# Kernel tuning notes

Hardware: AMD Instinct MI355X
Metric: run time of the kernel (lower is better)

The kernel has to match this reference:

```python
import jax, jax.numpy as jnp
import numpy as np
import math

S, B, D_MODEL = 1024, 2, 1024
N_HEADS = 16
D_HEAD = D_MODEL // N_HEADS
C = 32  # compressed_len


def _xavier(key, shape):
    fan_in, fan_out = shape[-1], shape[-2] if len(shape) > 1 else shape[-1]
    limit = math.sqrt(6.0 / (fan_in + fan_out))
    return jax.random.uniform(key, shape, jnp.float32, -limit, limit)


def setup_inputs() -> dict:
    key = jax.random.key(0)
    ks = jax.random.split(key, 10)
    return {
        "x": jax.random.normal(ks[0], (S, B, D_MODEL), jnp.float32),
        "q_down": _xavier(ks[1], (C, D_MODEL)),
        "Wq": _xavier(ks[2], (D_MODEL, D_MODEL)),
        "bq": jnp.zeros((D_MODEL,), jnp.float32),
        "Wk": _xavier(ks[3], (D_MODEL, D_MODEL)),
        "bk": jnp.zeros((D_MODEL,), jnp.float32),
        "Wv": _xavier(ks[4], (D_MODEL, D_MODEL)),
        "bv": jnp.zeros((D_MODEL,), jnp.float32),
        "Wo": _xavier(ks[5], (D_MODEL, D_MODEL)),
        "bo": jnp.zeros((D_MODEL,), jnp.float32),
    }


def reference(x, q_down, Wq, bq, Wk, bk, Wv, bv, Wo, bo):
    # x: (s, b, d_model); causal=True, rope=None, dropout inactive (eval)
    s, b, d_model = x.shape
    h, dh = N_HEADS, D_HEAD
    scale = 1.0 / math.sqrt(dh)

    q_u = x @ Wq.T + bq                       # (s,b,dm)
    k_d = x @ Wk.T + bk
    v_d = x @ Wv.T + bv
    v_d_k = v_d @ Wk.T + bk
    v_d_v = v_d @ Wv.T + bv

    def heads(t):  # (s,b,dm) -> (b,h,s,dh)
        return t.reshape(s, b, h, dh).transpose(1, 2, 0, 3)

    q_u = heads(q_u) * scale
    k_d = heads(k_d)
    v_d_kv = jnp.concatenate([heads(v_d_k), heads(v_d_v)], axis=-1)  # (b,h,s,2dh)

    q_d = q_down.reshape(C, h, dh).transpose(1, 0, 2) * scale        # (h,c,dh)

    down = jnp.einsum('hcd,bhsd->bhcs', q_d, k_d)                    # (b,h,c,s)
    w = jnp.exp(down - jnp.max(down, axis=-1, keepdims=True))
    norm = jnp.cumsum(w, axis=-1)

    # (b,h,c,s,2dh): running compressed KV state
    kv_u = jnp.cumsum(w[..., None] * v_d_kv[:, :, None, :, :], axis=3) / norm[..., None]
    k_u, v_u = jnp.split(kv_u, 2, axis=-1)                           # each (b,h,c,s,dh)

    up = jnp.einsum('bhsd,bhcsd->bhsc', q_u, k_u)
    up = jax.nn.softmax(up, axis=-1)
    out = jnp.einsum('bhsc,bhcsd->bhsd', up, v_u)                    # (b,h,s,dh)

    out = out.transpose(2, 0, 1, 3).reshape(s, b, d_model)
    return out @ Wo.T + bo
```

## Files before the change

### kernel.cpp

```cpp
#include <hip/hip_runtime.h>
#include <cstdint>
#include <cstddef>

#define S_LEN 1024
#define BATCH 2
#define DM    1024
#define NH    16
#define DH    64
#define CC    32
#define SB    2048
#define TSD   128
#define NCHD  8

using short8 = __attribute__((ext_vector_type(8))) short;
using f32x4  = __attribute__((ext_vector_type(4))) float;

__device__ __forceinline__ float b2f(unsigned short u) {
    union { unsigned int i; float f; } v; v.i = ((unsigned int)u) << 16; return v.f;
}
__device__ __forceinline__ unsigned short f2b(float f) {
    union { float f; unsigned int i; } v; v.f = f;
    unsigned int x = v.i;
    unsigned int r = x + 0x7FFFu + ((x >> 16) & 1u);
    return (unsigned short)(r >> 16);
}

__device__ __forceinline__ void async_ld16(const unsigned short* g, unsigned short* l) {
    __builtin_amdgcn_global_load_lds(
        (const __attribute__((address_space(1))) unsigned int*)g,
        (__attribute__((address_space(3))) unsigned int*)l,
        16, 0, 0);
}

__global__ __launch_bounds__(256) void k_convert(
    const void* x, const void* qd,
    const void* wq, const void* wk, const void* wv,
    const void* bq, const void* bk, const void* bv, const void* bo,
    int* __restrict__ flag,
    unsigned short* xb, unsigned short* qdb,
    unsigned short* Wqb, unsigned short* Wkb, unsigned short* Wvb,
    float* biasf)
{
    __shared__ int cnt;
    if (threadIdx.x == 0) cnt = 0;
    __syncthreads();
    {
        const unsigned short* xs = (const unsigned short*)x;
        int local = 0;
        for (int i = threadIdx.x; i < 1024; i += 256) {
            unsigned e = (xs[i * 2] >> 7) & 0xFF;
            if (e >= 90 && e <= 160) local++;
        }
        atomicAdd(&cnt, local);
    }
    __syncthreads();
    const int isbf = (cnt >= 640);
    if (blockIdx.x == 0 && threadIdx.x == 0) *flag = isbf;

    const size_t tid = (size_t)blockIdx.x * 256 + threadIdx.x;
    const size_t stride = (size_t)gridDim.x * 256;

    if (!isbf) {
        auto cv = [&](const void* src, unsigned short* dst, size_t n) {
            const float4* s = (const float4*)src;
            for (size_t i = tid; i < n / 4; i += stride) {
                float4 v = s[i];
                ushort4 o;
                o.x = f2b(v.x); o.y = f2b(v.y); o.z = f2b(v.z); o.w = f2b(v.w);
                ((ushort4*)dst)[i] = o;
            }
        };
        cv(x,  xb,  (size_t)SB * DM);
        cv(qd, qdb, (size_t)CC * DM);
        cv(wq, Wqb, (size_t)DM * DM);
        cv(wk, Wkb, (size_t)DM * DM);
        cv(wv, Wvb, (size_t)DM * DM);
    }
    for (size_t i = tid; i < 5 * DM; i += stride) {
        int w = (int)(i >> 10), o = (int)(i & 1023);
        float val;
        if (w == 4) val = 0.f;
        else {
            const void* bp = (w == 0) ? bq : ((w == 1) ? bk : ((w == 2) ? bv : bo));
            val = isbf ? b2f(((const unsigned short*)bp)[o]) : ((const float*)bp)[o];
        }
        biasf[i] = val;
    }
}

struct GArg {
    const unsigned short* A0;
    const unsigned short* A1;
    const unsigned short* B0;
    const unsigned short* B1;
    const float* bias;
    void* out;
    float scale;
    int mode;
};

__global__ __launch_bounds__(256) void k_g1conv(
    GArg g0, GArg g1, GArg g2, const int* __restrict__ flag,
    int M, int N, int K,
    const void* __restrict__ wo_raw, unsigned short* __restrict__ Wob)
{
    const int isbf = *flag;
    const int t = threadIdx.x;

    if (blockIdx.z == 3) {
        if (!isbf) {
            const float4* s = (const float4*)wo_raw;
            const int id = blockIdx.y * 8 + blockIdx.x;
            for (int i = id * 256 + t; i < (DM * DM) / 4; i += 256 * 256) {
                float4 v = s[i];
                ushort4 o;
                o.x = f2b(v.x); o.y = f2b(v.y); o.z = f2b(v.z); o.w = f2b(v.w);
                ((ushort4*)Wob)[i] = o;
            }
        }
        return;
    }

    GArg ga = (blockIdx.z == 0) ? g0 : (blockIdx.z == 1) ? g1 : g2;
    const unsigned short* Ap = isbf ? ga.A1 : ga.A0;
    const unsigned short* Bp = isbf ? ga.B1 : ga.B0;
    const int m0 = blockIdx.y * 64;
    const int n0 = blockIdx.x * 128;
    __shared__ __align__(16) unsigned short As[2][64 * 32];
    __shared__ __align__(16) unsigned short Bs[2][128 * 32];
    const int w = t >> 6, l = t & 63;
    const int wm = w >> 1, wn = w & 1;
    const int lr = l >> 2;
    const int lk = (l & 3) * 8;
    const int ln = l & 15;
    const int lq = l >> 4;

    f32x4 acc[2][4] = {};

    const unsigned short* Ab  = Ap + (size_t)(m0 + w * 16 +      lr) * K + lk;
    const unsigned short* Bb0 = Bp + (size_t)(n0 + w * 32 +      lr) * K + lk;
    const unsigned short* Bb1 = Bp + (size_t)(n0 + w * 32 + 16 + lr) * K + lk;

    for (int kk = 0; kk < K; kk += 64) {
#pragma unroll
        for (int hh = 0; hh < 2; ++hh) {
            async_ld16(Ab  + kk + hh * 32, &As[hh][w * 512]);
            async_ld16(Bb0 + kk + hh * 32, &Bs[hh][w * 1024]);
            async_ld16(Bb1 + kk + hh * 32, &Bs[hh][w * 1024 + 512]);
        }
        __syncthreads();
#pragma unroll
        for (int hh = 0; hh < 2; ++hh) {
            short8 af[2], bfr[4];
#pragma unroll
            for (int i = 0; i < 2; ++i)
                af[i] = *(const short8*)&As[hh][(wm * 32 + i * 16 + ln) * 32 + lq * 8];
#pragma unroll
            for (int j = 0; j < 4; ++j)
                bfr[j] = *(const short8*)&Bs[hh][(wn * 64 + j * 16 + ln) * 32 + lq * 8];
#pragma unroll
            for (int i = 0; i < 2; ++i)
#pragma unroll
                for (int j = 0; j < 4; ++j)
                    acc[i][j] = __builtin_amdgcn_mfma_f32_16x16x32_bf16(af[i], bfr[j], acc[i][j], 0, 0, 0);
        }
        __syncthreads();
    }

    const float sc = ga.scale;
#pragma unroll
    for (int j = 0; j < 4; ++j) {
        int col = n0 + wn * 64 + j * 16 + ln;
        float bv = ga.bias[col];
#pragma unroll
        for (int i = 0; i < 2; ++i) {
            int row0 = m0 + wm * 32 + i * 16 + lq * 4;
#pragma unroll
            for (int r = 0; r < 4; ++r) {
                float v = (acc[i][j][r] + bv) * sc;
                ((unsigned short*)ga.out)[(size_t)(row0 + r) * N + col] = f2b(v);
            }
        }
    }
}

__global__ __launch_bounds__(256) void gemm_f64(GArg ga,
                                                const int* __restrict__ flag,
                                                int M, int N, int K)
{
    const int isbf = *flag;
    const unsigned short* Ap = isbf ? ga.A1 : ga.A0;
    const unsigned short* Bp = isbf ? ga.B1 : ga.B0;
    const int m0 = blockIdx.y * 64;
    const int n0 = blockIdx.x * 64;
    __shared__ __align__(16) unsigned short As[2][64 * 32];
    __shared__ __align__(16) unsigned short Bs[2][64 * 32];
    const int t = threadIdx.x;
    const int w = t >> 6, l = t & 63;
    const int wm = w >> 1, wn = w & 1;
    const int lr = l >> 2;
    const int lk = (l & 3) * 8;
    const int ln = l & 15;
    const int lq = l >> 4;

    f32x4 acc[2][2] = {};

    const unsigned short* Ab = Ap + (size_t)(m0 + w * 16 + lr) * K + lk;
    const unsigned short* Bb = Bp + (size_t)(n0 + w * 16 + lr) * K + lk;

    for (int kk = 0; kk < K; kk += 64) {
#pragma unroll
        for (int hh = 0; hh < 2; ++hh) {
            async_ld16(Ab + kk + hh * 32, &As[hh][w * 512]);
            async_ld16(Bb + kk + hh * 32, &Bs[hh][w * 512]);
        }
        __syncthreads();
#pragma unroll
        for (int hh = 0; hh < 2; ++hh) {
            short8 af[2], bfr[2];
#pragma unroll
            for (int i = 0; i < 2; ++i)
                af[i] = *(const short8*)&As[hh][(wm * 32 + i * 16 + ln) * 32 + lq * 8];
#pragma unroll
            for (int j = 0; j < 2; ++j)
                bfr[j] = *(const short8*)&Bs[hh][(wn * 32 + j * 16 + ln) * 32 + lq * 8];
#pragma unroll
            for (int i = 0; i < 2; ++i)
#pragma unroll
                for (int j = 0; j < 2; ++j)
                    acc[i][j] = __builtin_amdgcn_mfma_f32_16x16x32_bf16(af[i], bfr[j], acc[i][j], 0, 0, 0);
        }
        __syncthreads();
    }

    const int f32o = (ga.mode == 0) ? 1 : (ga.mode == 1) ? 0 : (!isbf);
    const float sc = ga.scale;
#pragma unroll
    for (int j = 0; j < 2; ++j) {
        int col = n0 + wn * 32 + j * 16 + ln;
        float bv = ga.bias[col];
#pragma unroll
        for (int i = 0; i < 2; ++i) {
            int row0 = m0 + wm * 32 + i * 16 + lq * 4;
#pragma unroll
            for (int r = 0; r < 4; ++r) {
                float v = (acc[i][j][r] + bv) * sc;
                size_t idx = (size_t)(row0 + r) * N + col;
                if (f32o) ((float*)ga.out)[idx] = v;
                else      ((unsigned short*)ga.out)[idx] = f2b(v);
            }
        }
    }
}

__global__ __launch_bounds__(256) void k_g2down(
    GArg g0, GArg g1, const int* __restrict__ flag, int M, int N, int K,
    const unsigned short* __restrict__ kd,
    const unsigned short* __restrict__ qd0,
    const unsigned short* __restrict__ qd1,
    float* __restrict__ wbuf,
    float* __restrict__ cmax,
    float* __restrict__ csum)
{
    __shared__ __align__(16) unsigned char SM[40448];
    const int isbf = *flag;
    const int t = threadIdx.x;
    const int w = t >> 6, l = t & 63;
    const int ln = l & 15, lq = l >> 4;

    if (blockIdx.z < 2) {
        unsigned short* As = (unsigned short*)SM;
        unsigned short* Bs = (unsigned short*)(SM + 8192);
        GArg ga = blockIdx.z ? g1 : g0;
        const unsigned short* Ap = isbf ? ga.A1 : ga.A0;
        const unsigned short* Bp = isbf ? ga.B1 : ga.B0;
        const int m0 = blockIdx.y * 64;
        const int n0 = blockIdx.x * 128;
        const int wm = w >> 1, wn = w & 1;
        const int lr = l >> 2;
        const int lk = (l & 3) * 8;

        f32x4 acc[2][4] = {};

        const unsigned short* Ab  = Ap + (size_t)(m0 + w * 16 +      lr) * K + lk;
        const unsigned short* Bb0 = Bp + (size_t)(n0 + w * 32 +      lr) * K + lk;
        const unsigned short* Bb1 = Bp + (size_t)(n0 + w * 32 + 16 + lr) * K + lk;

        for (int kk = 0; kk < K; kk += 64) {
#pragma unroll
            for (int hh = 0; hh < 2; ++hh) {
                async_ld16(Ab  + kk + hh * 32, &As[hh * 2048 + w * 512]);
                async_ld16(Bb0 + kk + hh * 32, &Bs[hh * 4096 + w * 1024]);
                async_ld16(Bb1 + kk + hh * 32, &Bs[hh * 4096 + w * 1024 + 512]);
            }
            __syncthreads();
#pragma unroll
            for (int hh = 0; hh < 2; ++hh) {
                short8 af[2], bfr[4];
#pragma unroll
                for (int i = 0; i < 2; ++i)
                    af[i] = *(const short8*)&As[hh * 2048 + (wm * 32 + i * 16 + ln) * 32 + lq * 8];
#pragma unroll
                for (int j = 0; j < 4; ++j)
                    bfr[j] = *(const short8*)&Bs[hh * 4096 + (wn * 64 + j * 16 + ln) * 32 + lq * 8];
#pragma unroll
                for (int i = 0; i < 2; ++i)
#pragma unroll
                    for (int j = 0; j < 4; ++j)
                        acc[i][j] = __builtin_amdgcn_mfma_f32_16x16x32_bf16(af[i], bfr[j], acc[i][j], 0, 0, 0);
            }
            __syncthreads();
        }

        const float sc = ga.scale;
#pragma unroll
        for (int j = 0; j < 4; ++j) {
            int col = n0 + wn * 64 + j * 16 + ln;
            float bv = ga.bias[col];
#pragma unroll
            for (int i = 0; i < 2; ++i) {
                int row0 = m0 + wm * 32 + i * 16 + lq * 4;
#pragma unroll
                for (int r = 0; r < 4; ++r) {
                    float v = (acc[i][j][r] + bv) * sc;
                    ((unsigned short*)ga.out)[(size_t)(row0 + r) * N + col] = f2b(v);
                }
            }
        }
    } else {
        unsigned short* QD = (unsigned short*)SM;
        unsigned short* KT = (unsigned short*)(SM + 4608);
        float* SS          = (float*)(SM + 23040);
        float* cmf         = (float*)(SM + 39936);

        const int id = blockIdx.y * 8 + blockIdx.x;
        const unsigned short* qdw = isbf ? qd1 : qd0;
        const int bh = id >> 3;
        const int b = bh >> 4, h = bh & 15;
        const int chunk = id & 7;
        const int s0 = chunk * TSD;

        {
            int r = t >> 3, cb = (t & 7) * 8;
            *(short8*)&QD[r * 72 + cb] = *(const short8*)&qdw[(size_t)r * DM + h * DH + cb];
        }
        for (int u = t; u < 128 * 8; u += 256) {
            int r = u >> 3, cb = (u & 7) * 8;
            *(short8*)&KT[r * 72 + cb] =
                *(const short8*)&kd[(size_t)((s0 + r) * BATCH + b) * DM + h * DH + cb];
        }
        __syncthreads();

        f32x4 accG[2][2] = {};
#pragma unroll
        for (int ks = 0; ks < 2; ++ks) {
            short8 a8[2], b8[2];
#pragma unroll
            for (int i = 0; i < 2; ++i)
                a8[i] = *(const short8*)&QD[(i * 16 + ln) * 72 + ks * 32 + lq * 8];
#pragma unroll
            for (int j = 0; j < 2; ++j)
                b8[j] = *(const short8*)&KT[(w * 32 + j * 16 + ln) * 72 + ks * 32 + lq * 8];
#pragma unroll
            for (int i = 0; i < 2; ++i)
#pragma unroll
                for (int j = 0; j < 2; ++j)
                    accG[i][j] = __builtin_amdgcn_mfma_f32_16x16x32_bf16(a8[i], b8[j], accG[i][j], 0, 0, 0);
        }
#pragma unroll
        for (int i = 0; i < 2; ++i) {
#pragma unroll
            for (int j = 0; j < 2; ++j) {
                int sl = w * 32 + j * 16 + ln;
#pragma unroll
                for (int r = 0; r < 4; ++r) {
                    int c = i * 16 + lq * 4 + r;
                    float v = accG[i][j][r] * 0.125f;
                    SS[c * 132 + sl] = v;
                    wbuf[((size_t)bh * CC + c) * S_LEN + s0 + sl] = v;
                }
            }
        }
        __syncthreads();

        const int c = t >> 3, sub = t & 7;
        float lmax = -3.4e38f;
#pragma unroll
        for (int k = 0; k < 16; ++k) lmax = fmaxf(lmax, SS[c * 132 + sub * 16 + k]);
        lmax = fmaxf(lmax, __shfl_xor(lmax, 1));
        lmax = fmaxf(lmax, __shfl_xor(lmax, 2));
        lmax = fmaxf(lmax, __shfl_xor(lmax, 4));
        if (sub == 0) {
            cmf[c] = lmax;
            cmax[((size_t)bh * CC + c) * NCHD + chunk] = lmax;
        }
        __syncthreads();
        const float cm = cmf[c];
        float es = 0.f;
#pragma unroll
        for (int k = 0; k < 16; ++k) es += __expf(SS[c * 132 + sub * 16 + k] - cm);
        es += __shfl_xor(es, 1);
        es += __shfl_xor(es, 2);
        es += __shfl_xor(es, 4);
        if (sub == 0) csum[((size_t)bh * CC + c) * NCHD + chunk] = es;
    }
}

__global__ __launch_bounds__(256) void k_wstate(
    const float* __restrict__ wbuf,
    const float* __restrict__ cmax,
    const float* __restrict__ csum,
    const unsigned short* __restrict__ vdk,
    const unsigned short* __restrict__ vdv,
    unsigned short* __restrict__ wb,
    float* __restrict__ invn,
    float* __restrict__ Mst,
    float* __restrict__ NTst)
{
    __shared__ __align__(16) unsigned char SM[45568];
    unsigned short* Wfull = (unsigned short*)SM;
    unsigned char* R = SM + 8704;
    float* gm    = (float*)R;
    float* basep = (float*)(R + 128);
    float* psum  = (float*)(R + 256);
    float* invt  = (float*)(R + 1408);
    unsigned short* T1 = (unsigned short*)R;
    unsigned short* T2 = (unsigned short*)(R + 9216);
    unsigned short* KT = (unsigned short*)(R + 18432);
    unsigned short* VT = (unsigned short*)(R + 27648);

    const int bh = blockIdx.x, seg = blockIdx.y;
    const int b = bh >> 4, h = bh & 15;
    const int t = threadIdx.x;
    const int w = t >> 6, l = t & 63;
    const int ln = l & 15, lq = l >> 4;

    if (t < CC) {
        const size_t cb = (size_t)(bh * CC + t) * NCHD;
        float m = cmax[cb];
#pragma unroll
        for (int g = 1; g < NCHD; ++g) m = fmaxf(m, cmax[cb + g]);
        gm[t] = m;
        float bsum = 0.f;
        for (int k = 0; k < seg; ++k)
            bsum += csum[cb + k] * __expf(cmax[cb + k] - m);
        basep[t] = bsum;
    }
    __syncthreads();

    {
        const int c = t >> 3, sub = t & 7;
        const float gmc = gm[c];
        const size_t rbase = (size_t)bh * 32768 + c * 1024 + seg * 128 + sub * 16;
        float w16[16];
        float s = 0.f;
#pragma unroll
        for (int i = 0; i < 16; ++i) {
            float v = __expf(wbuf[rbase + i] - gmc);
            w16[i] = v; s += v;
        }
        psum[c * 9 + sub] = s;
        short8 o0, o1;
#pragma unroll
        for (int i = 0; i < 8; ++i) { o0[i] = f2b(w16[i]); o1[i] = f2b(w16[8 + i]); }
        *(short8*)&wb[rbase] = o0;
        *(short8*)&wb[rbase + 8] = o1;
        *(short8*)&Wfull[c * 136 + sub * 16] = o0;
        *(short8*)&Wfull[c * 136 + sub * 16 + 8] = o1;
        __syncthreads();

        float run = basep[c];
        for (int k = 0; k < sub; ++k) run += psum[c * 9 + k];
#pragma unroll
        for (int i = 0; i < 16; ++i) {
            run += w16[i];
            invt[(sub * 16 + i) * 36 + c] = 1.0f / fmaxf(run, 1e-30f);
        }
    }
    __syncthreads();

    for (int u = t; u < 128 * 8; u += 256) {
        int r = u >> 3, cb2 = (u & 7) * 4;
        *(float4*)&invn[(size_t)bh * 32768 + (seg * 128 + r) * 32 + cb2] =
            *(const float4*)&invt[r * 36 + cb2];
    }
    __syncthreads();

    for (int rep = 0; rep < 2; ++rep) {
        const int ch = seg * 2 + rep;
        const int s0 = ch * 64;

        for (int u = t; u < 64 * 8; u += 256) {
            int r = u >> 3, cb = (u & 7) * 8;
            *(short8*)&T1[r * 72 + cb] =
                *(const short8*)&vdk[(size_t)((s0 + r) * BATCH + b) * DM + h * DH + cb];
            *(short8*)&T2[r * 72 + cb] =
                *(const short8*)&vdv[(size_t)((s0 + r) * BATCH + b) * DM + h * DH + cb];
        }
        __syncthreads();
        for (int u = t; u < 64 * 8; u += 256) {
            int d = u >> 3, s8 = (u & 7) * 8;
            short8 o1, o2;
#pragma unroll
            for (int k = 0; k < 8; ++k) {
                o1[k] = T1[(s8 + k) * 72 + d];
                o2[k] = T2[(s8 + k) * 72 + d];
            }
            *(short8*)&KT[d * 72 + s8] = o1;
            *(short8*)&VT[d * 72 + s8] = o2;
        }
        __syncthreads();

        f32x4 accM[2] = {};
#pragma unroll
        for (int ks = 0; ks < 2; ++ks) {
            short8 b8 = *(const short8*)&KT[(w * 16 + ln) * 72 + ks * 32 + lq * 8];
#pragma unroll
            for (int i = 0; i < 2; ++i) {
                short8 a8 = *(const short8*)&Wfull[(i * 16 + ln) * 136 + rep * 64 + ks * 32 + lq * 8];
                accM[i] = __builtin_amdgcn_mfma_f32_16x16x32_bf16(a8, b8, accM[i], 0, 0, 0);
            }
        }
#pragma unroll
        for (int i = 0; i < 2; ++i)
#pragma unroll
            for (int r = 0; r < 4; ++r)
                Mst[((size_t)(bh * 16 + ch) * 32 + i * 16 + lq * 4 + r) * 64 + w * 16 + ln] = accM[i][r];

        f32x4 accN[2] = {};
#pragma unroll
        for (int ks = 0; ks < 2; ++ks) {
            short8 a8 = *(const short8*)&VT[(w * 16 + ln) * 72 + ks * 32 + lq * 8];
#pragma unroll
            for (int j = 0; j < 2; ++j) {
                short8 b8 = *(const short8*)&Wfull[(j * 16 + ln) * 136 + rep * 64 + ks * 32 + lq * 8];
                accN[j] = __builtin_amdgcn_mfma_f32_16x16x32_bf16(a8, b8, accN[j], 0, 0, 0);
            }
        }
#pragma unroll
        for (int j = 0; j < 2; ++j)
#pragma unroll
            for (int r = 0; r < 4; ++r)
                NTst[((size_t)(bh * 16 + ch) * 64 + w * 16 + lq * 4 + r) * 32 + j * 16 + ln] = accN[j][r];
        __syncthreads();
    }
}

__global__ __launch_bounds__(256) void k_att(
    const unsigned short* __restrict__ qu,
    const unsigned short* __restrict__ vdk,
    const unsigned short* __restrict__ wb,
    const float* __restrict__ invn,
    const unsigned short* __restrict__ vdv,
    const float* __restrict__ Mst,
    const float* __restrict__ NTst,
    unsigned short* __restrict__ attout)
{
    const int bh = blockIdx.x, b = bh >> 4, h = bh & 15;
    const int qi = blockIdx.y;
    const int s0 = qi * 64;
    const int t = threadIdx.x;
    const int w = t >> 6, l = t & 63;
    const int wy = w >> 1, wx = w & 1;
    const int ln = l & 15, lq = l >> 4;

    __shared__ __align__(16) unsigned short Qs[64 * 72];
    __shared__ __align__(16) unsigned short Gs[64 * 72];
    __shared__ __align__(16) unsigned short Kd[64 * 72];
    __shared__ __align__(16) unsigned short Wd[32 * 72];
    __shared__ __align__(16) unsigned short WTd[64 * 40];
    __shared__ __align__(16) unsigned short VTd[64 * 72];
    __shared__ __align__(16) unsigned short Mc[32 * 72];
    __shared__ __align__(16) unsigned short Nc[64 * 40];

    for (int u = t; u < 64 * 8; u += 256) {
        int r = u >> 3, cb = (u & 7) * 8;
        *(short8*)&Qs[r * 72 + cb] =
            *(const short8*)&qu[(size_t)(s0 + r) * 2048 + b * 1024 + h * 64 + cb];
        *(short8*)&Kd[r * 72 + cb] =
            *(const short8*)&vdk[(size_t)(s0 + r) * 2048 + b * 1024 + h * 64 + cb];
        *(short8*)&Gs[r * 72 + cb] =
            *(const short8*)&vdv[(size_t)(s0 + r) * 2048 + b * 1024 + h * 64 + cb];
    }
    for (int u = t; u < 32 * 8; u += 256) {
        int r = u >> 3, cb = (u & 7) * 8;
        *(short8*)&Wd[r * 72 + cb] =
            *(const short8*)&wb[(size_t)bh * 32768 + r * 1024 + s0 + cb];
    }
    {
        float am[8] = {0.f, 0.f, 0.f, 0.f, 0.f, 0.f, 0.f, 0.f};
        float an[8] = {0.f, 0.f, 0.f, 0.f, 0.f, 0.f, 0.f, 0.f};
        for (int ch = 0; ch < qi; ++ch) {
            const float* pm = Mst + ((size_t)(bh * 16 + ch)) * 2048 + t * 8;
            const float* pn = NTst + ((size_t)(bh * 16 + ch)) * 2048 + t * 8;
            float4 m0 = *(const float4*)pm;
            float4 m1 = *(const float4*)(pm + 4);
            float4 n0 = *(const float4*)pn;
            float4 n1 = *(const float4*)(pn + 4);
            am[0] += m0.x; am[1] += m0.y; am[2] += m0.z; am[3] += m0.w;
            am[4] += m1.x; am[5] += m1.y; am[6] += m1.z; am[7] += m1.w;
            an[0] += n0.x; an[1] += n0.y; an[2] += n0.z; an[3] += n0.w;
            an[4] += n1.x; an[5] += n1.y; an[6] += n1.z; an[7] += n1.w;
        }
        short8 mo, no;
#pragma unroll
        for (int j = 0; j < 8; ++j) { mo[j] = f2b(am[j]); no[j] = f2b(an[j]); }
        *(short8*)&Mc[(t >> 3) * 72 + (t & 7) * 8] = mo;
        *(short8*)&Nc[(t >> 2) * 40 + (t & 3) * 8] = no;
    }
    __syncthreads();

    for (int u = t; u < 64 * 8; u += 256) {
        int d = u >> 3, s8 = (u & 7) * 8;
        short8 o;
#pragma unroll
        for (int k = 0; k < 8; ++k) o[k] = Gs[(s8 + k) * 72 + d];
        *(short8*)&VTd[d * 72 + s8] = o;
    }
    {
        int sl = t >> 2, cb = (t & 3) * 8;
        short8 o;
#pragma unroll
        for (int k = 0; k < 8; ++k) o[k] = Wd[(cb + k) * 72 + sl];
        *(short8*)&WTd[sl * 40 + cb] = o;
    }
    __syncthreads();

    {
        f32x4 accG[2][2] = {};
#pragma unroll
        for (int ks = 0; ks < 2; ++ks) {
            short8 a8[2], b8[2];
#pragma unroll
            for (int i = 0; i < 2; ++i)
                a8[i] = *(const short8*)&Qs[(wy * 32 + i * 16 + ln) * 72 + ks * 32 + lq * 8];
#pragma unroll
            for (int j = 0; j < 2; ++j)
                b8[j] = *(const short8*)&Kd[(wx * 32 + j * 16 + ln) * 72 + ks * 32 + lq * 8];
#pragma unroll
            for (int i = 0; i < 2; ++i)
#pragma unroll
                for (int j = 0; j < 2; ++j)
                    accG[i][j] = __builtin_amdgcn_mfma_f32_16x16x32_bf16(a8[i], b8[j], accG[i][j], 0, 0, 0);
        }
        __syncthreads();
#pragma unroll
        for (int i = 0; i < 2; ++i) {
            int row = wy * 32 + i * 16 + lq * 4;
#pragma unroll
            for (int j = 0; j < 2; ++j) {
                int col = wx * 32 + j * 16 + ln;
#pragma unroll
                for (int r = 0; r < 4; ++r) {
                    float v = accG[i][j][r];
                    if (col > row + r) v = 0.f;
                    Gs[(row + r) * 72 + col] = f2b(v);
                }
            }
        }
    }
    __syncthreads();

    f32x4 accU[2] = {};
#pragma unroll
    for (int ks = 0; ks < 2; ++ks) {
        short8 ga = *(const short8*)&Gs[(w * 16 + ln) * 72 + ks * 32 + lq * 8];
        short8 qa = *(const short8*)&Qs[(w * 16 + ln) * 72 + ks * 32 + lq * 8];
#pragma unroll
        for (int j = 0; j < 2; ++j) {
            short8 wf = *(const short8*)&Wd[(j * 16 + ln) * 72 + ks * 32 + lq * 8];
            short8 mf = *(const short8*)&Mc[(j * 16 + ln) * 72 + ks * 32 + lq * 8];
            accU[j] = __builtin_amdgcn_mfma_f32_16x16x32_bf16(ga, wf, accU[j], 0, 0, 0);
            accU[j] = __builtin_amdgcn_mfma_f32_16x16x32_bf16(qa, mf, accU[j], 0, 0, 0);
        }
    }
    __syncthreads();

    {
        int rowl = w * 16 + lq * 4;
#pragma unroll
        for (int r = 0; r < 4; ++r) {
            int srow = s0 + rowl + r;
            float inv0 = invn[(size_t)bh * 32768 + srow * 32 + ln];
            float inv1 = invn[(size_t)bh * 32768 + srow * 32 + 16 + ln];
            float l0 = accU[0][r] * inv0;
            float l1 = accU[1][r] * inv1;
            float m = fmaxf(l0, l1);
#pragma unroll
            for (int msk = 1; msk < 16; msk <<= 1) m = fmaxf(m, __shfl_xor(m, msk));
            float e0 = __expf(l0 - m), e1 = __expf(l1 - m);
            float Z = e0 + e1;
#pragma unroll
            for (int msk = 1; msk < 16; msk <<= 1) Z += __shfl_xor(Z, msk);
            float iz = 1.0f / Z;
            Qs[(rowl + r) * 40 + ln]      = f2b(e0 * iz * inv0);
            Qs[(rowl + r) * 40 + 16 + ln] = f2b(e1 * iz * inv1);
        }
    }
    __syncthreads();

    short8 pa[2];
#pragma unroll
    for (int i = 0; i < 2; ++i)
        pa[i] = *(const short8*)&Qs[(wy * 32 + i * 16 + ln) * 40 + lq * 8];
    {
        f32x4 accS[2][2] = {};
        short8 b8[2];
#pragma unroll
        for (int j = 0; j < 2; ++j)
            b8[j] = *(const short8*)&WTd[(wx * 32 + j * 16 + ln) * 40 + lq * 8];
#pragma unroll
        for (int i = 0; i < 2; ++i)
#pragma unroll
            for (int j = 0; j < 2; ++j)
                accS[i][j] = __builtin_amdgcn_mfma_f32_16x16x32_bf16(pa[i], b8[j], accS[i][j], 0, 0, 0);
#pragma unroll
        for (int i = 0; i < 2; ++i) {
            int row = wy * 32 + i * 16 + lq * 4;
#pragma unroll
            for (int j = 0; j < 2; ++j) {
                int col = wx * 32 + j * 16 + ln;
#pragma unroll
                for (int r = 0; r < 4; ++r) {
                    float v = accS[i][j][r];
                    if (col > row + r) v = 0.f;
                    Gs[(row + r) * 72 + col] = f2b(v);
                }
            }
        }
    }
    __syncthreads();

    {
        f32x4 accO[2][2] = {};
        short8 n8[2];
#pragma unroll
        for (int j = 0; j < 2; ++j)
            n8[j] = *(const short8*)&Nc[(wx * 32 + j * 16 + ln) * 40 + lq * 8];
#pragma unroll
        for (int i = 0; i < 2; ++i)
#pragma unroll
            for (int j = 0; j < 2; ++j)
                accO[i][j] = __builtin_amdgcn_mfma_f32_16x16x32_bf16(pa[i], n8[j], accO[i][j], 0, 0, 0);
#pragma unroll
        for (int ks = 0; ks < 2; ++ks) {
            short8 a8[2], b8[2];
#pragma unroll
            for (int i = 0; i < 2; ++i)
                a8[i] = *(const short8*)&Gs[(wy * 32 + i * 16 + ln) * 72 + ks * 32 + lq * 8];
#pragma unroll
            for (int j = 0; j < 2; ++j)
                b8[j] = *(const short8*)&VTd[(wx * 32 + j * 16 + ln) * 72 + ks * 32 + lq * 8];
#pragma unroll
            for (int i = 0; i < 2; ++i)
#pragma unroll
                for (int j = 0; j < 2; ++j)
                    accO[i][j] = __builtin_amdgcn_mfma_f32_16x16x32_bf16(a8[i], b8[j], accO[i][j], 0, 0, 0);
        }
#pragma unroll
        for (int i = 0; i < 2; ++i) {
            int rowb = s0 + wy * 32 + i * 16 + lq * 4;
#pragma unroll
            for (int j = 0; j < 2; ++j) {
                int d = wx * 32 + j * 16 + ln;
#pragma unroll
                for (int r = 0; r < 4; ++r)
                    attout[(size_t)(rowb + r) * 2048 + b * 1024 + h * 64 + d] = f2b(accO[i][j][r]);
            }
        }
    }
}

extern "C" void kernel_launch(void* const* d_in, const int* in_sizes, int n_in,
                              void* d_out, int out_size, void* d_ws, size_t ws_size,
                              hipStream_t stream)
{
    (void)in_sizes; (void)n_in; (void)out_size; (void)ws_size;
    char* ws = (char*)d_ws;
    const size_t MB = (size_t)1 << 20;
    const size_t KB = (size_t)1 << 10;
    unsigned short* attout = (unsigned short*)(ws + 0 * MB);
    unsigned short* q_u    = (unsigned short*)(ws + 4 * MB);
    unsigned short* k_d    = (unsigned short*)(ws + 8 * MB);
    unsigned short* v_dk   = (unsigned short*)(ws + 12 * MB);
    unsigned short* v_dv   = (unsigned short*)(ws + 16 * MB);
    float* wbuf = (float*)(ws + 20 * MB);
    unsigned short* wb  = (unsigned short*)(ws + 24 * MB);
    float* invn = (float*)(ws + 28 * MB);
    float* Mst  = (float*)(ws + 32 * MB);
    float* NTst = (float*)(ws + 36 * MB);
    unsigned short* xb  = (unsigned short*)(ws + 44 * MB);
    unsigned short* Wqb = (unsigned short*)(ws + 48 * MB);
    unsigned short* Wkb = (unsigned short*)(ws + 50 * MB);
    unsigned short* Wvb = (unsigned short*)(ws + 52 * MB);
    unsigned short* Wob = (unsigned short*)(ws + 54 * MB);
    unsigned short* v_d = (unsigned short*)(ws + 56 * MB);
    unsigned short* qdb = (unsigned short*)(ws + 62 * MB);
    float* biasf  = (float*)(ws + 62 * MB + 64 * KB);
    float* cmax   = (float*)(ws + 62 * MB + 192 * KB);
    float* csum   = (float*)(ws + 62 * MB + 256 * KB);
    int*   flag   = (int*)  (ws + 62 * MB + 320 * KB);

    const unsigned short* xraw  = (const unsigned short*)d_in[0];
    const unsigned short* qdraw = (const unsigned short*)d_in[1];
    const unsigned short* wqraw = (const unsigned short*)d_in[2];
    const unsigned short* wkraw = (const unsigned short*)d_in[4];
    const unsigned short* wvraw = (const unsigned short*)d_in[6];
    const unsigned short* woraw = (const unsigned short*)d_in[8];

    k_convert<<<1024, 256, 0, stream>>>(
        d_in[0], d_in[1], d_in[2], d_in[4], d_in[6],
        d_in[3], d_in[5], d_in[7], d_in[9],
        flag, xb, qdb, Wqb, Wkb, Wvb, biasf);

    const float* bqf = biasf;
    const float* bkf = biasf + 1024;
    const float* bvf = biasf + 2048;
    const float* bof = biasf + 3072;

    GArg gq { xb, xraw, Wqb, wqraw, bqf, (void*)q_u, 0.125f, 1 };
    GArg gk { xb, xraw, Wkb, wkraw, bkf, (void*)k_d, 1.0f, 1 };
    GArg gv { xb, xraw, Wvb, wvraw, bvf, (void*)v_d, 1.0f, 1 };
    k_g1conv<<<dim3(8, 32, 4), 256, 0, stream>>>(gq, gk, gv, flag, SB, DM, DM,
                                                 d_in[8], Wob);

    GArg gvk{ v_d, v_d, Wkb, wkraw, bkf, (void*)v_dk, 1.0f, 1 };
    GArg gvv{ v_d, v_d, Wvb, wvraw, bvf, (void*)v_dv, 1.0f, 1 };
    k_g2down<<<dim3(8, 32, 3), 256, 0, stream>>>(gvk, gvv, flag, SB, DM, DM,
                                                 k_d, qdb, qdraw, wbuf, cmax, csum);

    k_wstate<<<dim3(32, 8), 256, 0, stream>>>(wbuf, cmax, csum, v_dk, v_dv,
                                              wb, invn, Mst, NTst);
    k_att<<<dim3(32, 16), 256, 0, stream>>>(q_u, v_dk, wb, invn, v_dv,
                                            Mst, NTst, attout);

    GArg go{ attout, attout, Wob, woraw, bof, d_out, 1.0f, 2 };
    gemm_f64<<<dim3(16, 32), 256, 0, stream>>>(go, flag, SB, DM, DM);
}
```

Before: 164.5 us.

## Fuse fp32-to-bf16 input conversion into GEMM tile loads and drop convert kernel

```diff
diff --git a/kernel.cpp b/kernel.cpp
--- a/kernel.cpp
+++ b/kernel.cpp
@@ -32,85 +32,52 @@
         16, 0, 0);
 }
 
-__global__ __launch_bounds__(256) void k_convert(
-    const void* x, const void* qd,
-    const void* wq, const void* wk, const void* wv,
-    const void* bq, const void* bk, const void* bv, const void* bo,
-    int* __restrict__ flag,
-    unsigned short* xb, unsigned short* qdb,
-    unsigned short* Wqb, unsigned short* Wkb, unsigned short* Wvb,
-    float* biasf)
-{
-    __shared__ int cnt;
-    if (threadIdx.x == 0) cnt = 0;
-    __syncthreads();
-    {
-        const unsigned short* xs = (const unsigned short*)x;
-        int local = 0;
-        for (int i = threadIdx.x; i < 1024; i += 256) {
-            unsigned e = (xs[i * 2] >> 7) & 0xFF;
-            if (e >= 90 && e <= 160) local++;
-        }
-        atomicAdd(&cnt, local);
-    }
-    __syncthreads();
-    const int isbf = (cnt >= 640);
-    if (blockIdx.x == 0 && threadIdx.x == 0) *flag = isbf;
-
-    const size_t tid = (size_t)blockIdx.x * 256 + threadIdx.x;
-    const size_t stride = (size_t)gridDim.x * 256;
-
-    if (!isbf) {
-        auto cv = [&](const void* src, unsigned short* dst, size_t n) {
-            const float4* s = (const float4*)src;
-            for (size_t i = tid; i < n / 4; i += stride) {
-                float4 v = s[i];
-                ushort4 o;
-                o.x = f2b(v.x); o.y = f2b(v.y); o.z = f2b(v.z); o.w = f2b(v.w);
-                ((ushort4*)dst)[i] = o;
-            }
-        };
-        cv(x,  xb,  (size_t)SB * DM);
-        cv(qd, qdb, (size_t)CC * DM);
-        cv(wq, Wqb, (size_t)DM * DM);
-        cv(wk, Wkb, (size_t)DM * DM);
-        cv(wv, Wvb, (size_t)DM * DM);
-    }
-    for (size_t i = tid; i < 5 * DM; i += stride) {
-        int w = (int)(i >> 10), o = (int)(i & 1023);
-        float val;
-        if (w == 4) val = 0.f;
-        else {
-            const void* bp = (w == 0) ? bq : ((w == 1) ? bk : ((w == 2) ? bv : bo));
-            val = isbf ? b2f(((const unsigned short*)bp)[o]) : ((const float*)bp)[o];
-        }
-        biasf[i] = val;
-    }
-}
-
-struct GArg {
-    const unsigned short* A0;
-    const unsigned short* A1;
-    const unsigned short* B0;
-    const unsigned short* B1;
-    const float* bias;
-    void* out;
+__device__ __forceinline__ short8 cvt8(const float* s) {
+    float4 v0 = *(const float4*)s;
+    float4 v1 = *(const float4*)(s + 4);
+    short8 o;
+    o[0] = f2b(v0.x); o[1] = f2b(v0.y); o[2] = f2b(v0.z); o[3] = f2b(v0.w);
+    o[4] = f2b(v1.x); o[5] = f2b(v1.y); o[6] = f2b(v1.z); o[7] = f2b(v1.w);
+    return o;
+}
+
+__device__ __forceinline__ int sniff_isbf(const unsigned short* xs) {
+    const int l = threadIdx.x & 63;
+    int local = 0;
+    for (int i = l; i < 1024; i += 64) {
+        unsigned e = (xs[i * 2] >> 7) & 0xFF;
+        if (e >= 90 && e <= 160) local++;
+    }
+#pragma unroll
+    for (int m = 1; m < 64; m <<= 1) local += __shfl_xor(local, m);
+    return local >= 640;
+}
+
+__device__ __forceinline__ float bias_at(const void* bias, int col, int isbf) {
+    return isbf ? b2f(((const unsigned short*)bias)[col]) : ((const float*)bias)[col];
+}
+
+struct G1 {
+    const void* B;
+    const void* bias;
+    unsigned short* out;
     float scale;
-    int mode;
 };
 
 __global__ __launch_bounds__(256) void k_g1conv(
-    GArg g0, GArg g1, GArg g2, const int* __restrict__ flag,
-    int M, int N, int K,
+    const void* __restrict__ x, G1 g0, G1 g1, G1 g2,
+    int* __restrict__ flag_out,
     const void* __restrict__ wo_raw, unsigned short* __restrict__ Wob)
 {
-    const int isbf = *flag;
+    const unsigned short* xs = (const unsigned short*)x;
+    const int isbf = sniff_isbf(xs);
     const int t = threadIdx.x;
 
     if (blockIdx.z == 3) {
+        const int id = blockIdx.y * 8 + blockIdx.x;
+        if (id == 0 && t == 0) *flag_out = isbf;
         if (!isbf) {
             const float4* s = (const float4*)wo_raw;
-            const int id = blockIdx.y * 8 + blockIdx.x;
             for (int i = id * 256 + t; i < (DM * DM) / 4; i += 256 * 256) {
                 float4 v = s[i];
                 ushort4 o;
@@ -121,9 +88,7 @@
         return;
     }
 
-    GArg ga = (blockIdx.z == 0) ? g0 : (blockIdx.z == 1) ? g1 : g2;
-    const unsigned short* Ap = isbf ? ga.A1 : ga.A0;
-    const unsigned short* Bp = isbf ? ga.B1 : ga.B0;
+    G1 ga = (blockIdx.z == 0) ? g0 : (blockIdx.z == 1) ? g1 : g2;
     const int m0 = blockIdx.y * 64;
     const int n0 = blockIdx.x * 128;
     __shared__ __align__(16) unsigned short As[2][64 * 32];
@@ -137,60 +102,97 @@
 
     f32x4 acc[2][4] = {};
 
-    const unsigned short* Ab  = Ap + (size_t)(m0 + w * 16 +      lr) * K + lk;
-    const unsigned short* Bb0 = Bp + (size_t)(n0 + w * 32 +      lr) * K + lk;
-    const unsigned short* Bb1 = Bp + (size_t)(n0 + w * 32 + 16 + lr) * K + lk;
-
-    for (int kk = 0; kk < K; kk += 64) {
-#pragma unroll
-        for (int hh = 0; hh < 2; ++hh) {
-            async_ld16(Ab  + kk + hh * 32, &As[hh][w * 512]);
-            async_ld16(Bb0 + kk + hh * 32, &Bs[hh][w * 1024]);
-            async_ld16(Bb1 + kk + hh * 32, &Bs[hh][w * 1024 + 512]);
-        }
-        __syncthreads();
-#pragma unroll
-        for (int hh = 0; hh < 2; ++hh) {
-            short8 af[2], bfr[4];
-#pragma unroll
-            for (int i = 0; i < 2; ++i)
-                af[i] = *(const short8*)&As[hh][(wm * 32 + i * 16 + ln) * 32 + lq * 8];
-#pragma unroll
-            for (int j = 0; j < 4; ++j)
-                bfr[j] = *(const short8*)&Bs[hh][(wn * 64 + j * 16 + ln) * 32 + lq * 8];
-#pragma unroll
-            for (int i = 0; i < 2; ++i)
+    const int row_a  = m0 + w * 16 + lr;
+    const int row_b0 = n0 + w * 32 + lr;
+    const int row_b1 = row_b0 + 16;
+
+    if (isbf) {
+        const unsigned short* Ab  = xs + (size_t)row_a * DM + lk;
+        const unsigned short* Bb0 = (const unsigned short*)ga.B + (size_t)row_b0 * DM + lk;
+        const unsigned short* Bb1 = (const unsigned short*)ga.B + (size_t)row_b1 * DM + lk;
+        for (int kk = 0; kk < DM; kk += 64) {
+#pragma unroll
+            for (int hh = 0; hh < 2; ++hh) {
+                async_ld16(Ab  + kk + hh * 32, &As[hh][w * 512]);
+                async_ld16(Bb0 + kk + hh * 32, &Bs[hh][w * 1024]);
+                async_ld16(Bb1 + kk + hh * 32, &Bs[hh][w * 1024 + 512]);
+            }
+            __syncthreads();
+#pragma unroll
+            for (int hh = 0; hh < 2; ++hh) {
+                short8 af[2], bfr[4];
+#pragma unroll
+                for (int i = 0; i < 2; ++i)
+                    af[i] = *(const short8*)&As[hh][(wm * 32 + i * 16 + ln) * 32 + lq * 8];
 #pragma unroll
                 for (int j = 0; j < 4; ++j)
-                    acc[i][j] = __builtin_amdgcn_mfma_f32_16x16x32_bf16(af[i], bfr[j], acc[i][j], 0, 0, 0);
-        }
-        __syncthreads();
+                    bfr[j] = *(const short8*)&Bs[hh][(wn * 64 + j * 16 + ln) * 32 + lq * 8];
+#pragma unroll
+                for (int i = 0; i < 2; ++i)
+#pragma unroll
+                    for (int j = 0; j < 4; ++j)
+                        acc[i][j] = __builtin_amdgcn_mfma_f32_16x16x32_bf16(af[i], bfr[j], acc[i][j], 0, 0, 0);
+            }
+            __syncthreads();
+        }
+    } else {
+        const float* Af  = (const float*)x    + (size_t)row_a  * DM + lk;
+        const float* Bf0 = (const float*)ga.B + (size_t)row_b0 * DM + lk;
+        const float* Bf1 = (const float*)ga.B + (size_t)row_b1 * DM + lk;
+        for (int kk = 0; kk < DM; kk += 64) {
+#pragma unroll
+            for (int hh = 0; hh < 2; ++hh) {
+                *(short8*)&As[hh][w * 512  + l * 8]       = cvt8(Af  + kk + hh * 32);
+                *(short8*)&Bs[hh][w * 1024 + l * 8]       = cvt8(Bf0 + kk + hh * 32);
+                *(short8*)&Bs[hh][w * 1024 + 512 + l * 8] = cvt8(Bf1 + kk + hh * 32);
+            }
+            __syncthreads();
+#pragma unroll
+            for (int hh = 0; hh < 2; ++hh) {
+                short8 af[2], bfr[4];
+#pragma unroll
+                for (int i = 0; i < 2; ++i)
+                    af[i] = *(const short8*)&As[hh][(wm * 32 + i * 16 + ln) * 32 + lq * 8];
+#pragma unroll
+                for (int j = 0; j < 4; ++j)
+                    bfr[j] = *(const short8*)&Bs[hh][(wn * 64 + j * 16 + ln) * 32 + lq * 8];
+#pragma unroll
+                for (int i = 0; i < 2; ++i)
+#pragma unroll
+                    for (int j = 0; j < 4; ++j)
+                        acc[i][j] = __builtin_amdgcn_mfma_f32_16x16x32_bf16(af[i], bfr[j], acc[i][j], 0, 0, 0);
+            }
+            __syncthreads();
+        }
     }
 
     const float sc = ga.scale;
 #pragma unroll
     for (int j = 0; j < 4; ++j) {
         int col = n0 + wn * 64 + j * 16 + ln;
-        float bv = ga.bias[col];
+        float bv = bias_at(ga.bias, col, isbf);
 #pragma unroll
         for (int i = 0; i < 2; ++i) {
             int row0 = m0 + wm * 32 + i * 16 + lq * 4;
 #pragma unroll
             for (int r = 0; r < 4; ++r) {
                 float v = (acc[i][j][r] + bv) * sc;
-                ((unsigned short*)ga.out)[(size_t)(row0 + r) * N + col] = f2b(v);
-            }
-        }
-    }
-}
-
-__global__ __launch_bounds__(256) void gemm_f64(GArg ga,
-                                                const int* __restrict__ flag,
-                                                int M, int N, int K)
+                ga.out[(size_t)(row0 + r) * DM + col] = f2b(v);
+            }
+        }
+    }
+}
+
+__global__ __launch_bounds__(256) void gemm_f64(
+    const unsigned short* __restrict__ A,
+    const unsigned short* __restrict__ B0,
+    const unsigned short* __restrict__ B1,
+    const void* __restrict__ bo,
+    const int* __restrict__ flag,
+    void* __restrict__ out)
 {
     const int isbf = *flag;
-    const unsigned short* Ap = isbf ? ga.A1 : ga.A0;
-    const unsigned short* Bp = isbf ? ga.B1 : ga.B0;
+    const unsigned short* Bp = isbf ? B1 : B0;
     const int m0 = blockIdx.y * 64;
     const int n0 = blockIdx.x * 64;
     __shared__ __align__(16) unsigned short As[2][64 * 32];
@@ -205,10 +207,10 @@
 
     f32x4 acc[2][2] = {};
 
-    const unsigned short* Ab = Ap + (size_t)(m0 + w * 16 + lr) * K + lk;
-    const unsigned short* Bb = Bp + (size_t)(n0 + w * 16 + lr) * K + lk;
-
-    for (int kk = 0; kk < K; kk += 64) {
+    const unsigned short* Ab = A  + (size_t)(m0 + w * 16 + lr) * DM + lk;
+    const unsigned short* Bb = Bp + (size_t)(n0 + w * 16 + lr) * DM + lk;
+
+    for (int kk = 0; kk < DM; kk += 64) {
 #pragma unroll
         for (int hh = 0; hh < 2; ++hh) {
             async_ld16(Ab + kk + hh * 32, &As[hh][w * 512]);
@@ -233,31 +235,36 @@
         __syncthreads();
     }
 
-    const int f32o = (ga.mode == 0) ? 1 : (ga.mode == 1) ? 0 : (!isbf);
-    const float sc = ga.scale;
+    const int f32o = !isbf;
 #pragma unroll
     for (int j = 0; j < 2; ++j) {
         int col = n0 + wn * 32 + j * 16 + ln;
-        float bv = ga.bias[col];
+        float bv = bias_at(bo, col, isbf);
 #pragma unroll
         for (int i = 0; i < 2; ++i) {
             int row0 = m0 + wm * 32 + i * 16 + lq * 4;
 #pragma unroll
             for (int r = 0; r < 4; ++r) {
-                float v = (acc[i][j][r] + bv) * sc;
-                size_t idx = (size_t)(row0 + r) * N + col;
-                if (f32o) ((float*)ga.out)[idx] = v;
-                else      ((unsigned short*)ga.out)[idx] = f2b(v);
-            }
-        }
-    }
-}
+                float v = acc[i][j][r] + bv;
+                size_t idx = (size_t)(row0 + r) * DM + col;
+                if (f32o) ((float*)out)[idx] = v;
+                else      ((unsigned short*)out)[idx] = f2b(v);
+            }
+        }
+    }
+}
+
+struct G2 {
+    const void* B;
+    const void* bias;
+    unsigned short* out;
+};
 
 __global__ __launch_bounds__(256) void k_g2down(
-    GArg g0, GArg g1, const int* __restrict__ flag, int M, int N, int K,
+    const unsigned short* __restrict__ vd, G2 g0, G2 g1,
+    const int* __restrict__ flag,
     const unsigned short* __restrict__ kd,
-    const unsigned short* __restrict__ qd0,
-    const unsigned short* __restrict__ qd1,
+    const void* __restrict__ qd_raw,
     float* __restrict__ wbuf,
     float* __restrict__ cmax,
     float* __restrict__ csum)
@@ -271,9 +278,7 @@
     if (blockIdx.z < 2) {
         unsigned short* As = (unsigned short*)SM;
         unsigned short* Bs = (unsigned short*)(SM + 8192);
-        GArg ga = blockIdx.z ? g1 : g0;
-        const unsigned short* Ap = isbf ? ga.A1 : ga.A0;
-        const unsigned short* Bp = isbf ? ga.B1 : ga.B0;
+        G2 ga = blockIdx.z ? g1 : g0;
         const int m0 = blockIdx.y * 64;
         const int n0 = blockIdx.x * 128;
         const int wm = w >> 1, wn = w & 1;
@@ -282,48 +287,79 @@
 
         f32x4 acc[2][4] = {};
 
-        const unsigned short* Ab  = Ap + (size_t)(m0 + w * 16 +      lr) * K + lk;
-        const unsigned short* Bb0 = Bp + (size_t)(n0 + w * 32 +      lr) * K + lk;
-        const unsigned short* Bb1 = Bp + (size_t)(n0 + w * 32 + 16 + lr) * K + lk;
-
-        for (int kk = 0; kk < K; kk += 64) {
-#pragma unroll
-            for (int hh = 0; hh < 2; ++hh) {
-                async_ld16(Ab  + kk + hh * 32, &As[hh * 2048 + w * 512]);
-                async_ld16(Bb0 + kk + hh * 32, &Bs[hh * 4096 + w * 1024]);
-                async_ld16(Bb1 + kk + hh * 32, &Bs[hh * 4096 + w * 1024 + 512]);
-            }
-            __syncthreads();
-#pragma unroll
-            for (int hh = 0; hh < 2; ++hh) {
-                short8 af[2], bfr[4];
-#pragma unroll
-                for (int i = 0; i < 2; ++i)
-                    af[i] = *(const short8*)&As[hh * 2048 + (wm * 32 + i * 16 + ln) * 32 + lq * 8];
-#pragma unroll
-                for (int j = 0; j < 4; ++j)
-                    bfr[j] = *(const short8*)&Bs[hh * 4096 + (wn * 64 + j * 16 + ln) * 32 + lq * 8];
-#pragma unroll
-                for (int i = 0; i < 2; ++i)
+        const int row_b0 = n0 + w * 32 + lr;
+        const int row_b1 = row_b0 + 16;
+        const unsigned short* Ab = vd + (size_t)(m0 + w * 16 + lr) * DM + lk;
+
+        if (isbf) {
+            const unsigned short* Bb0 = (const unsigned short*)ga.B + (size_t)row_b0 * DM + lk;
+            const unsigned short* Bb1 = (const unsigned short*)ga.B + (size_t)row_b1 * DM + lk;
+            for (int kk = 0; kk < DM; kk += 64) {
+#pragma unroll
+                for (int hh = 0; hh < 2; ++hh) {
+                    async_ld16(Ab  + kk + hh * 32, &As[hh * 2048 + w * 512]);
+                    async_ld16(Bb0 + kk + hh * 32, &Bs[hh * 4096 + w * 1024]);
+                    async_ld16(Bb1 + kk + hh * 32, &Bs[hh * 4096 + w * 1024 + 512]);
+                }
+                __syncthreads();
+#pragma unroll
+                for (int hh = 0; hh < 2; ++hh) {
+                    short8 af[2], bfr[4];
+#pragma unroll
+                    for (int i = 0; i < 2; ++i)
+                        af[i] = *(const short8*)&As[hh * 2048 + (wm * 32 + i * 16 + ln) * 32 + lq * 8];
 #pragma unroll
                     for (int j = 0; j < 4; ++j)
-                        acc[i][j] = __builtin_amdgcn_mfma_f32_16x16x32_bf16(af[i], bfr[j], acc[i][j], 0, 0, 0);
-            }
-            __syncthreads();
-        }
-
-        const float sc = ga.scale;
+                        bfr[j] = *(const short8*)&Bs[hh * 4096 + (wn * 64 + j * 16 + ln) * 32 + lq * 8];
+#pragma unroll
+                    for (int i = 0; i < 2; ++i)
+#pragma unroll
+                        for (int j = 0; j < 4; ++j)
+                            acc[i][j] = __builtin_amdgcn_mfma_f32_16x16x32_bf16(af[i], bfr[j], acc[i][j], 0, 0, 0);
+                }
+                __syncthreads();
+            }
+        } else {
+            const float* Bf0 = (const float*)ga.B + (size_t)row_b0 * DM + lk;
+            const float* Bf1 = (const float*)ga.B + (size_t)row_b1 * DM + lk;
+            for (int kk = 0; kk < DM; kk += 64) {
+#pragma unroll
+                for (int hh = 0; hh < 2; ++hh) {
+                    async_ld16(Ab + kk + hh * 32, &As[hh * 2048 + w * 512]);
+                    *(short8*)&Bs[hh * 4096 + w * 1024 + l * 8]       = cvt8(Bf0 + kk + hh * 32);
+                    *(short8*)&Bs[hh * 4096 + w * 1024 + 512 + l * 8] = cvt8(Bf1 + kk + hh * 32);
+                }
+                __syncthreads();
+#pragma unroll
+                for (int hh = 0; hh < 2; ++hh) {
+                    short8 af[2], bfr[4];
+#pragma unroll
+                    for (int i = 0; i < 2; ++i)
+                        af[i] = *(const short8*)&As[hh * 2048 + (wm * 32 + i * 16 + ln) * 32 + lq * 8];
+#pragma unroll
+                    for (int j = 0; j < 4; ++j)
+                        bfr[j] = *(const short8*)&Bs[hh * 4096 + (wn * 64 + j * 16 + ln) * 32 + lq * 8];
+#pragma unroll
+                    for (int i = 0; i < 2; ++i)
+#pragma unroll
+                        for (int j = 0; j < 4; ++j)
+                            acc[i][j] = __builtin_amdgcn_mfma_f32_16x16x32_bf16(af[i], bfr[j], acc[i][j], 0, 0, 0);
+                }
+                __syncthreads();
+            }
+        }
+
 #pragma unroll
         for (int j = 0; j < 4; ++j) {
             int col = n0 + wn * 64 + j * 16 + ln;
-            float bv = ga.bias[col];
+            float bv = bias_at(ga.bias, col, isbf);
 #pragma unroll
             for (int i = 0; i < 2; ++i) {
                 int row0 = m0 + wm * 32 + i * 16 + lq * 4;
 #pragma unroll
                 for (int r = 0; r < 4; ++r) {
-                    float v = (acc[i][j][r] + bv) * sc;
-                    ((unsigned short*)ga.out)[(size_t)(row0 + r) * N + col] = f2b(v);
+                    float v = acc[i][j][r] + bv;
+                    ga.out[(size_t)(row0 + r) * DM + col] = f2b(v);
                 }
             }
         }
@@ -334,7 +370,6 @@
         float* cmf         = (float*)(SM + 39936);
 
         const int id = blockIdx.y * 8 + blockIdx.x;
-        const unsigned short* qdw = isbf ? qd1 : qd0;
         const int bh = id >> 3;
         const int b = bh >> 4, h = bh & 15;
         const int chunk = id & 7;
@@ -342,7 +377,13 @@
 
         {
             int r = t >> 3, cb = (t & 7) * 8;
-            *(short8*)&QD[r * 72 + cb] = *(const short8*)&qdw[(size_t)r * DM + h * DH + cb];
+            if (isbf) {
+                *(short8*)&QD[r * 72 + cb] =
+                    *(const short8*)&((const unsigned short*)qd_raw)[(size_t)r * DM + h * DH + cb];
+            } else {
+                *(short8*)&QD[r * 72 + cb] =
+                    cvt8((const float*)qd_raw + (size_t)r * DM + h * DH + cb);
+            }
         }
         for (int u = t; u < 128 * 8; u += 256) {
             int r = u >> 3, cb = (u & 7) * 8;
@@ -789,51 +830,29 @@
     float* invn = (float*)(ws + 28 * MB);
     float* Mst  = (float*)(ws + 32 * MB);
     float* NTst = (float*)(ws + 36 * MB);
-    unsigned short* xb  = (unsigned short*)(ws + 44 * MB);
-    unsigned short* Wqb = (unsigned short*)(ws + 48 * MB);
-    unsigned short* Wkb = (unsigned short*)(ws + 50 * MB);
-    unsigned short* Wvb = (unsigned short*)(ws + 52 * MB);
     unsigned short* Wob = (unsigned short*)(ws + 54 * MB);
     unsigned short* v_d = (unsigned short*)(ws + 56 * MB);
-    unsigned short* qdb = (unsigned short*)(ws + 62 * MB);
-    float* biasf  = (float*)(ws + 62 * MB + 64 * KB);
     float* cmax   = (float*)(ws + 62 * MB + 192 * KB);
     float* csum   = (float*)(ws + 62 * MB + 256 * KB);
     int*   flag   = (int*)  (ws + 62 * MB + 320 * KB);
 
-    const unsigned short* xraw  = (const unsigned short*)d_in[0];
-    const unsigned short* qdraw = (const unsigned short*)d_in[1];
-    const unsigned short* wqraw = (const unsigned short*)d_in[2];
-    const unsigned short* wkraw = (const unsigned short*)d_in[4];
-    const unsigned short* wvraw = (const unsigned short*)d_in[6];
-    const unsigned short* woraw = (const unsigned short*)d_in[8];
-
-    k_convert<<<1024, 256, 0, stream>>>(
-        d_in[0], d_in[1], d_in[2], d_in[4], d_in[6],
-        d_in[3], d_in[5], d_in[7], d_in[9],
-        flag, xb, qdb, Wqb, Wkb, Wvb, biasf);
-
-    const float* bqf = biasf;
-    const float* bkf = biasf + 1024;
-    const float* bvf = biasf + 2048;
-    const float* bof = biasf + 3072;
-
-    GArg gq { xb, xraw, Wqb, wqraw, bqf, (void*)q_u, 0.125f, 1 };
-    GArg gk { xb, xraw, Wkb, wkraw, bkf, (void*)k_d, 1.0f, 1 };
-    GArg gv { xb, xraw, Wvb, wvraw, bvf, (void*)v_d, 1.0f, 1 };
-    k_g1conv<<<dim3(8, 32, 4), 256, 0, stream>>>(gq, gk, gv, flag, SB, DM, DM,
-                                                 d_in[8], Wob);
-
-    GArg gvk{ v_d, v_d, Wkb, wkraw, bkf, (void*)v_dk, 1.0f, 1 };
-    GArg gvv{ v_d, v_d, Wvb, wvraw, bvf, (void*)v_dv, 1.0f, 1 };
-    k_g2down<<<dim3(8, 32, 3), 256, 0, stream>>>(gvk, gvv, flag, SB, DM, DM,
-                                                 k_d, qdb, qdraw, wbuf, cmax, csum);
+    G1 gq{ d_in[2], d_in[3], q_u, 0.125f };
+    G1 gk{ d_in[4], d_in[5], k_d, 1.0f };
+    G1 gv{ d_in[6], d_in[7], v_d, 1.0f };
+    k_g1conv<<<dim3(8, 32, 4), 256, 0, stream>>>(d_in[0], gq, gk, gv,
+                                                 flag, d_in[8], Wob);
+
+    G2 gvk{ d_in[4], d_in[5], v_dk };
+    G2 gvv{ d_in[6], d_in[7], v_dv };
+    k_g2down<<<dim3(8, 32, 3), 256, 0, stream>>>(v_d, gvk, gvv, flag,
+                                                 k_d, d_in[1], wbuf, cmax, csum);
 
     k_wstate<<<dim3(32, 8), 256, 0, stream>>>(wbuf, cmax, csum, v_dk, v_dv,
                                               wb, invn, Mst, NTst);
     k_att<<<dim3(32, 16), 256, 0, stream>>>(q_u, v_dk, wb, invn, v_dv,
                                             Mst, NTst, attout);
 
-    GArg go{ attout, attout, Wob, woraw, bof, d_out, 1.0f, 2 };
-    gemm_f64<<<dim3(16, 32), 256, 0, stream>>>(go, flag, SB, DM, DM);
-}
+    gemm_f64<<<dim3(16, 32), 256, 0, stream>>>(attout, Wob,
+                                               (const unsigned short*)d_in[8],
+                                               d_in[9], flag, d_out);
+}
```

Result: slower. 195.4 us (+18.8%).
